# Kernel tuning notes

Measured on AMD Instinct MI355X. Metric: run time of the kernel, lower is better.

The kernel has to match this reference:

```python
import jax, jax.numpy as jnp
import numpy as np

N, DIM_EMB, HIDDEN, OUT = 8192, 256, 128, 64


def setup_inputs() -> dict:
    key = jax.random.key(0)
    k1, k2, k3, k4 = jax.random.split(key, 4)
    x = jax.random.normal(k1, (N, DIM_EMB), dtype=jnp.float32)
    adj = jax.random.uniform(k2, (N, N), dtype=jnp.float32)
    # GraphConvolution params (Glorot-style init)
    s1 = 1.0 / np.sqrt(DIM_EMB)
    s2 = 1.0 / np.sqrt(HIDDEN)
    W1 = jax.random.uniform(k3, (DIM_EMB, HIDDEN), dtype=jnp.float32, minval=-s1, maxval=s1)
    b1 = jnp.zeros((HIDDEN,), dtype=jnp.float32)
    W2 = jax.random.uniform(k4, (HIDDEN, OUT), dtype=jnp.float32, minval=-s2, maxval=s2)
    b2 = jnp.zeros((OUT,), dtype=jnp.float32)
    return {"x": x, "adj": adj, "W1": W1, "b1": b1, "W2": W2, "b2": b2}


def _adj_hat(adj):
    # torch: adj.mm(diag(d)).t().mm(diag(d)) == diag(d) @ adj.T @ diag(d)
    # expressed as broadcast row/col scaling (no NxN diag matmuls)
    d = jnp.power(jnp.sum(adj, axis=1), -0.5)  # [N]
    return (adj * d[None, :]).T * d[None, :]


def reference(x, adj, W1, b1, W2, b2):
    A = _adj_hat(adj)                     # [N, N]
    h = A @ (x @ W1) + b1                 # GraphConvolution 1
    h = jax.nn.relu(h)                    # dropout is identity in eval
    out = A @ (h @ W2) + b2               # GraphConvolution 2
    return out
```

## Files before the change

### kernel.cpp

```cpp
#include <hip/hip_runtime.h>
#include <math.h>

typedef unsigned short u16;
typedef __attribute__((ext_vector_type(8))) short short8v;
typedef __attribute__((ext_vector_type(4))) float f32x4v;
typedef __attribute__((ext_vector_type(4))) unsigned short u16x4;

#define GLOAD_LDS16(src, dst)                                      \
  __builtin_amdgcn_global_load_lds(                                \
      (const __attribute__((address_space(1))) void*)(src),        \
      (__attribute__((address_space(3))) void*)(dst), 16, 0, 0)

__device__ __forceinline__ u16 f2bf(float f) {
  union { float f; unsigned u; } v; v.f = f;
  unsigned r = v.u + 0x7FFFu + ((v.u >> 16) & 1u);
  return (u16)(r >> 16);
}

__global__ __launch_bounds__(256) void k_adj(const float* __restrict__ adj,
                                             u16* __restrict__ adjT,
                                             float* __restrict__ rsP) {
  __shared__ __align__(16) char Tsm[32768];
  const int tid = threadIdx.x, l = tid & 63, w = tid >> 6;
  const int c0 = blockIdx.x * 256, r0 = blockIdx.y * 64;
  for (int p = 0; p < 16; ++p) {
    const int rr = p * 4 + w;
    const float4 v = *(const float4*)(adj + (size_t)(r0 + rr) * 8192 + c0 + l * 4);
    float s = v.x + v.y + v.z + v.w;
#pragma unroll
    for (int off = 32; off > 0; off >>= 1) s += __shfl_xor(s, off, 64);
    if (l == 0) rsP[(size_t)blockIdx.x * 8192 + r0 + rr] = s;
    const float vv[4] = {v.x, v.y, v.z, v.w};
#pragma unroll
    for (int j = 0; j < 4; ++j) {
      const int c = l * 4 + j;
      const int phys = c * 128 + ((((rr >> 3) ^ (l & 7)) << 4) | ((rr & 7) << 1));
      *(u16*)(Tsm + phys) = f2bf(vv[j]);
    }
  }
  __syncthreads();
#pragma unroll
  for (int it = 0; it < 8; ++it) {
    const int chunk = it * 256 + tid;
    const int c = chunk >> 3, part = chunk & 7;
    const int pc = part ^ ((c >> 2) & 7);
    const float4 v = *(const float4*)(Tsm + c * 128 + pc * 16);
    *(float4*)((char*)adjT + ((size_t)(c0 + c) * 8192 + r0 + part * 8) * 2) = v;
  }
}

__global__ __launch_bounds__(256) void k_d(const float* __restrict__ rsP,
                                           float* __restrict__ dv) {
  const int i = blockIdx.x * 256 + threadIdx.x;
  float s = 0.f;
#pragma unroll
  for (int cx = 0; cx < 32; ++cx) s += rsP[(size_t)cx * 8192 + i];
  dv[i] = 1.0f / sqrtf(s);
}

__global__ __launch_bounds__(256) void k_prepw(const float* __restrict__ W1,
                                               const float* __restrict__ W2,
                                               u16* __restrict__ W1T,
                                               u16* __restrict__ W2T) {
  const int gid = blockIdx.x * 256 + threadIdx.x;
  { const int n = gid >> 8, c = gid & 255; W1T[gid] = f2bf(W1[c * 128 + n]); }
  if (gid < 8192) { const int n = gid >> 7, c = gid & 127; W2T[gid] = f2bf(W2[c * 64 + n]); }
}

__global__ __launch_bounds__(256) void k_convx(const float4* __restrict__ x,
                                               u16x4* __restrict__ xbf) {
  const int gid = blockIdx.x * 256 + threadIdx.x;
  const float4 v = x[gid];
  u16x4 o; o.x = f2bf(v.x); o.y = f2bf(v.y); o.z = f2bf(v.z); o.w = f2bf(v.w);
  xbf[gid] = o;
}

template <int BN, int EPI>
__global__ __launch_bounds__(256, 2) void gemm_kern(
    const u16* __restrict__ A, const u16* __restrict__ B,
    const float* __restrict__ dvec, float* __restrict__ Cp, u16* __restrict__ Ut,
    const int lda, const int ldb, const int ksteps) {
  constexpr int NREP = BN / 32;
  __shared__ __align__(16) u16 smem[16384 + 2 * BN * 64];
  const int tid = threadIdx.x, l = tid & 63, w = tid >> 6;
  const int wm = w >> 1, wn = w & 1;
  const int m0 = blockIdx.x * 128;
  const int kbase = blockIdx.y * ksteps * 64;
  const u16* Ag = A + (size_t)m0 * lda + kbase;
  const u16* Bg = B + kbase;
  u16* Asm = smem;
  u16* Bsm = smem + 16384;

  f32x4v acc[4][NREP];
  const f32x4v zero = {0.f, 0.f, 0.f, 0.f};
#pragma unroll
  for (int mr = 0; mr < 4; ++mr)
#pragma unroll
    for (int nr = 0; nr < NREP; ++nr) acc[mr][nr] = zero;

  auto stageA = [&](int k0, int buf) {
#pragma unroll
    for (int q = 0; q < 4; ++q) {
      const int c = q * 256 + tid;
      const int row = c >> 3;
      const int kp = (c & 7) ^ (row & 7);
      const u16* src = Ag + (size_t)row * lda + k0 + kp * 8;
      u16* dst = Asm + buf * 8192 + (q * 256 + (tid & ~63)) * 8;
      GLOAD_LDS16(src, dst);
    }
  };
  auto stageB = [&](int k0, int buf) {
#pragma unroll
    for (int q = 0; q < BN / 32; ++q) {
      const int c = q * 256 + tid;
      const int row = c >> 3;
      const int kp = (c & 7) ^ (row & 7);
      const u16* src = Bg + (size_t)row * ldb + k0 + kp * 8;
      u16* dst = Bsm + buf * (BN * 64) + (q * 256 + (tid & ~63)) * 8;
      GLOAD_LDS16(src, dst);
    }
  };

  stageA(0, 0);
  stageB(0, 0);

  for (int t = 0; t < ksteps; ++t) {
    const int cur = t & 1;
    __syncthreads();
    if (t + 1 < ksteps) { stageA((t + 1) * 64, cur ^ 1); stageB((t + 1) * 64, cur ^ 1); }
    const char* Ab = (const char*)(Asm + cur * 8192);
    const char* Bb = (const char*)(Bsm + cur * (BN * 64));
#pragma unroll
    for (int kk = 0; kk < 2; ++kk) {
      short8v a[4], b[NREP];
#pragma unroll
      for (int mr = 0; mr < 4; ++mr) {
        const int row = wm * 64 + mr * 16 + (l & 15);
        const int kb = kk * 64 + ((l >> 4) << 4);
        a[mr] = *(const short8v*)(Ab + row * 128 + (kb ^ ((row & 7) << 4)));
      }
#pragma unroll
      for (int nr = 0; nr < NREP; ++nr) {
        const int row = wn * (BN / 2) + nr * 16 + (l & 15);
        const int kb = kk * 64 + ((l >> 4) << 4);
        b[nr] = *(const short8v*)(Bb + row * 128 + (kb ^ ((row & 7) << 4)));
      }
#pragma unroll
      for (int mr = 0; mr < 4; ++mr)
#pragma unroll
        for (int nr = 0; nr < NREP; ++nr)
          acc[mr][nr] = __builtin_amdgcn_mfma_f32_16x16x32_bf16(a[mr], b[nr],
                                                                acc[mr][nr], 0, 0, 0);
    }
  }

  if (EPI == 0) {
    float* outp = Cp + (size_t)blockIdx.y * ((size_t)8192 * BN);
#pragma unroll
    for (int mr = 0; mr < 4; ++mr)
#pragma unroll
      for (int r = 0; r < 4; ++r) {
        const int m = m0 + wm * 64 + mr * 16 + ((l >> 4) << 2) + r;
#pragma unroll
        for (int nr = 0; nr < NREP; ++nr) {
          const int n = wn * (BN / 2) + nr * 16 + (l & 15);
          outp[(size_t)m * BN + n] = acc[mr][nr][r];
        }
      }
  } else {
    __syncthreads();
    u16* T = smem;
#pragma unroll
    for (int mr = 0; mr < 4; ++mr)
#pragma unroll
      for (int r = 0; r < 4; ++r) {
        const int mloc = wm * 64 + mr * 16 + ((l >> 4) << 2) + r;
        const float dd = dvec[m0 + mloc];
#pragma unroll
        for (int nr = 0; nr < NREP; ++nr) {
          const int n = wn * (BN / 2) + nr * 16 + (l & 15);
          T[n * 136 + mloc] = f2bf(acc[mr][nr][r] * dd);
        }
      }
    __syncthreads();
#pragma unroll
    for (int it = 0; it < BN / 16; ++it) {
      const int chunk = it * 256 + tid;
      const int n = chunk >> 4, part = chunk & 15;
      const float4 v = *(const float4*)(T + n * 136 + part * 8);
      *(float4*)((char*)Ut + ((size_t)n * 8192 + m0 + part * 8) * 2) = v;
    }
  }
}

__global__ __launch_bounds__(256) void k_e1(const float4* __restrict__ P,
                                            const float* __restrict__ dv,
                                            const float* __restrict__ b1,
                                            u16x4* __restrict__ h) {
  const int gid = blockIdx.x * 256 + threadIdx.x;
  const int STR = 262144;
  const float4 s0 = P[gid], s1 = P[gid + STR], s2 = P[gid + 2 * STR], s3 = P[gid + 3 * STR];
  const float dd = dv[gid >> 5];
  const float4 bb = ((const float4*)b1)[gid & 31];
  u16x4 o;
  o.x = f2bf(fmaxf(fmaf(dd, s0.x + s1.x + s2.x + s3.x, bb.x), 0.f));
  o.y = f2bf(fmaxf(fmaf(dd, s0.y + s1.y + s2.y + s3.y, bb.y), 0.f));
  o.z = f2bf(fmaxf(fmaf(dd, s0.z + s1.z + s2.z + s3.z, bb.z), 0.f));
  o.w = f2bf(fmaxf(fmaf(dd, s0.w + s1.w + s2.w + s3.w, bb.w), 0.f));
  h[gid] = o;
}

__global__ __launch_bounds__(256) void k_e2(const float4* __restrict__ P,
                                            const float* __restrict__ dv,
                                            const float* __restrict__ b2,
                                            float4* __restrict__ out) {
  const int gid = blockIdx.x * 256 + threadIdx.x;
  const int STR = 131072;
  const float4 s0 = P[gid], s1 = P[gid + STR], s2 = P[gid + 2 * STR], s3 = P[gid + 3 * STR];
  const float dd = dv[gid >> 4];
  const float4 bb = ((const float4*)b2)[gid & 15];
  float4 r;
  r.x = fmaf(dd, s0.x + s1.x + s2.x + s3.x, bb.x);
  r.y = fmaf(dd, s0.y + s1.y + s2.y + s3.y, bb.y);
  r.z = fmaf(dd, s0.z + s1.z + s2.z + s3.z, bb.z);
  r.w = fmaf(dd, s0.w + s1.w + s2.w + s3.w, bb.w);
  out[gid] = r;
}

extern "C" void kernel_launch(void* const* d_in, const int* in_sizes, int n_in,
                              void* d_out, int out_size, void* d_ws, size_t ws_size,
                              hipStream_t stream) {
  (void)in_sizes; (void)n_in; (void)out_size; (void)ws_size;
  const float* x   = (const float*)d_in[0];
  const float* adj = (const float*)d_in[1];
  const float* W1  = (const float*)d_in[2];
  const float* b1  = (const float*)d_in[3];
  const float* W2  = (const float*)d_in[4];
  const float* b2  = (const float*)d_in[5];
  float* out = (float*)d_out;
  char* ws = (char*)d_ws;

  u16*   adjT = (u16*)(ws + 0ull);
  float* T1p  = (float*)(ws + 134217728ull);
  float* T2p  = (float*)(ws + 151005184ull);
  u16*   xbf  = (u16*)(ws + 159393792ull);
  u16*   hbf  = (u16*)(ws + 163588096ull);
  u16*   U1T  = (u16*)(ws + 165685248ull);
  u16*   U2T  = (u16*)(ws + 167782400ull);
  u16*   W1T  = (u16*)(ws + 168830976ull);
  u16*   W2T  = (u16*)(ws + 168896512ull);
  float* rsP  = (float*)(ws + 168912896ull);
  float* dv   = (float*)(ws + 169961472ull);

  k_prepw<<<128, 256, 0, stream>>>(W1, W2, W1T, W2T);
  k_convx<<<2048, 256, 0, stream>>>((const float4*)x, (u16x4*)xbf);
  k_adj<<<dim3(32, 128), 256, 0, stream>>>(adj, adjT, rsP);
  k_d<<<32, 256, 0, stream>>>(rsP, dv);
  gemm_kern<128, 1><<<dim3(64, 1), 256, 0, stream>>>(xbf, W1T, dv, nullptr, U1T, 256, 256, 4);
  gemm_kern<128, 0><<<dim3(64, 4), 256, 0, stream>>>(adjT, U1T, nullptr, T1p, nullptr, 8192, 8192, 32);
  k_e1<<<1024, 256, 0, stream>>>((const float4*)T1p, dv, b1, (u16x4*)hbf);
  gemm_kern<64, 1><<<dim3(64, 1), 256, 0, stream>>>(hbf, W2T, dv, nullptr, U2T, 128, 128, 2);
  gemm_kern<64, 0><<<dim3(64, 4), 256, 0, stream>>>(adjT, U2T, nullptr, T2p, nullptr, 8192, 8192, 32);
  k_e2<<<512, 256, 0, stream>>>((const float4*)T2p, dv, b2, (float4*)out);
}
```

Baseline: 190.4 us.

## Shrink GEMM M-tile, batch adj loads, fuse prep kernels, reuse workspace

The GEMM kernel is templated on BM, and every launch now uses BM=64, which doubles the grid (128x4 instead of 64x4) to better fill the CUs at the cost of less A/B reuse per block. k_adj now issues 8 float4 loads before processing them, giving more memory-level parallelism. Its row-sum reduction is shortened to 16-lane groups, so partial sums grow to 128 slices, which k_d then reads. The weight-transpose and x-conversion kernels are merged into one launch, and the rsP buffer aliases T1p.

```diff
diff --git a/kernel.cpp b/kernel.cpp
--- a/kernel.cpp
+++ b/kernel.cpp
@@ -23,19 +23,30 @@
   __shared__ __align__(16) char Tsm[32768];
   const int tid = threadIdx.x, l = tid & 63, w = tid >> 6;
   const int c0 = blockIdx.x * 256, r0 = blockIdx.y * 64;
-  for (int p = 0; p < 16; ++p) {
-    const int rr = p * 4 + w;
-    const float4 v = *(const float4*)(adj + (size_t)(r0 + rr) * 8192 + c0 + l * 4);
-    float s = v.x + v.y + v.z + v.w;
-#pragma unroll
-    for (int off = 32; off > 0; off >>= 1) s += __shfl_xor(s, off, 64);
-    if (l == 0) rsP[(size_t)blockIdx.x * 8192 + r0 + rr] = s;
-    const float vv[4] = {v.x, v.y, v.z, v.w};
-#pragma unroll
-    for (int j = 0; j < 4; ++j) {
-      const int c = l * 4 + j;
-      const int phys = c * 128 + ((((rr >> 3) ^ (l & 7)) << 4) | ((rr & 7) << 1));
-      *(u16*)(Tsm + phys) = f2bf(vv[j]);
+  const int g = l >> 4;
+#pragma unroll
+  for (int pp = 0; pp < 2; ++pp) {
+    float4 v[8];
+#pragma unroll
+    for (int q = 0; q < 8; ++q) {
+      const int rr = (pp * 8 + q) * 4 + w;
+      v[q] = *(const float4*)(adj + (size_t)(r0 + rr) * 8192 + c0 + l * 4);
+    }
+#pragma unroll
+    for (int q = 0; q < 8; ++q) {
+      const int rr = (pp * 8 + q) * 4 + w;
+      float s = v[q].x + v[q].y + v[q].z + v[q].w;
+#pragma unroll
+      for (int off = 8; off > 0; off >>= 1) s += __shfl_xor(s, off, 64);
+      if ((l & 15) == 0)
+        rsP[(size_t)(blockIdx.x * 4 + g) * 8192 + r0 + rr] = s;
+      const float vv[4] = {v[q].x, v[q].y, v[q].z, v[q].w};
+#pragma unroll
+      for (int j = 0; j < 4; ++j) {
+        const int c = l * 4 + j;
+        const int phys = c * 128 + ((((rr >> 3) ^ (l & 7)) << 4) | ((rr & 7) << 1));
+        *(u16*)(Tsm + phys) = f2bf(vv[j]);
+      }
     }
   }
   __syncthreads();
@@ -53,59 +64,57 @@
                                            float* __restrict__ dv) {
   const int i = blockIdx.x * 256 + threadIdx.x;
   float s = 0.f;
-#pragma unroll
-  for (int cx = 0; cx < 32; ++cx) s += rsP[(size_t)cx * 8192 + i];
+#pragma unroll 8
+  for (int cx = 0; cx < 128; ++cx) s += rsP[(size_t)cx * 8192 + i];
   dv[i] = 1.0f / sqrtf(s);
 }
 
-__global__ __launch_bounds__(256) void k_prepw(const float* __restrict__ W1,
-                                               const float* __restrict__ W2,
-                                               u16* __restrict__ W1T,
-                                               u16* __restrict__ W2T) {
-  const int gid = blockIdx.x * 256 + threadIdx.x;
-  { const int n = gid >> 8, c = gid & 255; W1T[gid] = f2bf(W1[c * 128 + n]); }
-  if (gid < 8192) { const int n = gid >> 7, c = gid & 127; W2T[gid] = f2bf(W2[c * 64 + n]); }
-}
-
-__global__ __launch_bounds__(256) void k_convx(const float4* __restrict__ x,
-                                               u16x4* __restrict__ xbf) {
+__global__ __launch_bounds__(256) void k_prep(const float4* __restrict__ x,
+                                              u16x4* __restrict__ xbf,
+                                              const float* __restrict__ W1,
+                                              const float* __restrict__ W2,
+                                              u16* __restrict__ W1T,
+                                              u16* __restrict__ W2T) {
   const int gid = blockIdx.x * 256 + threadIdx.x;
   const float4 v = x[gid];
   u16x4 o; o.x = f2bf(v.x); o.y = f2bf(v.y); o.z = f2bf(v.z); o.w = f2bf(v.w);
   xbf[gid] = o;
-}
-
-template <int BN, int EPI>
+  if (gid < 32768) { const int n = gid >> 8, c = gid & 255; W1T[gid] = f2bf(W1[c * 128 + n]); }
+  if (gid < 8192)  { const int n = gid >> 7, c = gid & 127; W2T[gid] = f2bf(W2[c * 64 + n]); }
+}
+
+template <int BM, int BN, int EPI>
 __global__ __launch_bounds__(256, 2) void gemm_kern(
     const u16* __restrict__ A, const u16* __restrict__ B,
     const float* __restrict__ dvec, float* __restrict__ Cp, u16* __restrict__ Ut,
     const int lda, const int ldb, const int ksteps) {
+  constexpr int MREP = BM / 32;
   constexpr int NREP = BN / 32;
-  __shared__ __align__(16) u16 smem[16384 + 2 * BN * 64];
+  __shared__ __align__(16) u16 smem[2 * BM * 64 + 2 * BN * 64];
   const int tid = threadIdx.x, l = tid & 63, w = tid >> 6;
   const int wm = w >> 1, wn = w & 1;
-  const int m0 = blockIdx.x * 128;
+  const int m0 = blockIdx.x * BM;
   const int kbase = blockIdx.y * ksteps * 64;
   const u16* Ag = A + (size_t)m0 * lda + kbase;
   const u16* Bg = B + kbase;
   u16* Asm = smem;
-  u16* Bsm = smem + 16384;
-
-  f32x4v acc[4][NREP];
+  u16* Bsm = smem + 2 * BM * 64;
+
+  f32x4v acc[MREP][NREP];
   const f32x4v zero = {0.f, 0.f, 0.f, 0.f};
 #pragma unroll
-  for (int mr = 0; mr < 4; ++mr)
+  for (int mr = 0; mr < MREP; ++mr)
 #pragma unroll
     for (int nr = 0; nr < NREP; ++nr) acc[mr][nr] = zero;
 
   auto stageA = [&](int k0, int buf) {
 #pragma unroll
-    for (int q = 0; q < 4; ++q) {
+    for (int q = 0; q < BM / 32; ++q) {
       const int c = q * 256 + tid;
       const int row = c >> 3;
       const int kp = (c & 7) ^ (row & 7);
       const u16* src = Ag + (size_t)row * lda + k0 + kp * 8;
-      u16* dst = Asm + buf * 8192 + (q * 256 + (tid & ~63)) * 8;
+      u16* dst = Asm + buf * (BM * 64) + (q * 256 + (tid & ~63)) * 8;
       GLOAD_LDS16(src, dst);
     }
   };
@@ -128,14 +137,14 @@
     const int cur = t & 1;
     __syncthreads();
     if (t + 1 < ksteps) { stageA((t + 1) * 64, cur ^ 1); stageB((t + 1) * 64, cur ^ 1); }
-    const char* Ab = (const char*)(Asm + cur * 8192);
+    const char* Ab = (const char*)(Asm + cur * (BM * 64));
     const char* Bb = (const char*)(Bsm + cur * (BN * 64));
 #pragma unroll
     for (int kk = 0; kk < 2; ++kk) {
-      short8v a[4], b[NREP];
-#pragma unroll
-      for (int mr = 0; mr < 4; ++mr) {
-        const int row = wm * 64 + mr * 16 + (l & 15);
+      short8v a[MREP], b[NREP];
+#pragma unroll
+      for (int mr = 0; mr < MREP; ++mr) {
+        const int row = wm * (BM / 2) + mr * 16 + (l & 15);
         const int kb = kk * 64 + ((l >> 4) << 4);
         a[mr] = *(const short8v*)(Ab + row * 128 + (kb ^ ((row & 7) << 4)));
       }
@@ -146,7 +155,7 @@
         b[nr] = *(const short8v*)(Bb + row * 128 + (kb ^ ((row & 7) << 4)));
       }
 #pragma unroll
-      for (int mr = 0; mr < 4; ++mr)
+      for (int mr = 0; mr < MREP; ++mr)
 #pragma unroll
         for (int nr = 0; nr < NREP; ++nr)
           acc[mr][nr] = __builtin_amdgcn_mfma_f32_16x16x32_bf16(a[mr], b[nr],
@@ -157,10 +166,10 @@
   if (EPI == 0) {
     float* outp = Cp + (size_t)blockIdx.y * ((size_t)8192 * BN);
 #pragma unroll
-    for (int mr = 0; mr < 4; ++mr)
+    for (int mr = 0; mr < MREP; ++mr)
 #pragma unroll
       for (int r = 0; r < 4; ++r) {
-        const int m = m0 + wm * 64 + mr * 16 + ((l >> 4) << 2) + r;
+        const int m = m0 + wm * (BM / 2) + mr * 16 + ((l >> 4) << 2) + r;
 #pragma unroll
         for (int nr = 0; nr < NREP; ++nr) {
           const int n = wn * (BN / 2) + nr * 16 + (l & 15);
@@ -171,23 +180,23 @@
     __syncthreads();
     u16* T = smem;
 #pragma unroll
-    for (int mr = 0; mr < 4; ++mr)
+    for (int mr = 0; mr < MREP; ++mr)
 #pragma unroll
       for (int r = 0; r < 4; ++r) {
-        const int mloc = wm * 64 + mr * 16 + ((l >> 4) << 2) + r;
+        const int mloc = wm * (BM / 2) + mr * 16 + ((l >> 4) << 2) + r;
         const float dd = dvec[m0 + mloc];
 #pragma unroll
         for (int nr = 0; nr < NREP; ++nr) {
           const int n = wn * (BN / 2) + nr * 16 + (l & 15);
-          T[n * 136 + mloc] = f2bf(acc[mr][nr][r] * dd);
+          T[n * (BM + 8) + mloc] = f2bf(acc[mr][nr][r] * dd);
         }
       }
     __syncthreads();
 #pragma unroll
-    for (int it = 0; it < BN / 16; ++it) {
+    for (int it = 0; it < (BN * (BM / 8)) / 256; ++it) {
       const int chunk = it * 256 + tid;
-      const int n = chunk >> 4, part = chunk & 15;
-      const float4 v = *(const float4*)(T + n * 136 + part * 8);
+      const int n = chunk / (BM / 8), part = chunk & (BM / 8 - 1);
+      const float4 v = *(const float4*)(T + n * (BM + 8) + part * 8);
       *(float4*)((char*)Ut + ((size_t)n * 8192 + m0 + part * 8) * 2) = v;
     }
   }
@@ -249,17 +258,16 @@
   u16*   U2T  = (u16*)(ws + 167782400ull);
   u16*   W1T  = (u16*)(ws + 168830976ull);
   u16*   W2T  = (u16*)(ws + 168896512ull);
-  float* rsP  = (float*)(ws + 168912896ull);
-  float* dv   = (float*)(ws + 169961472ull);
-
-  k_prepw<<<128, 256, 0, stream>>>(W1, W2, W1T, W2T);
-  k_convx<<<2048, 256, 0, stream>>>((const float4*)x, (u16x4*)xbf);
+  float* dv   = (float*)(ws + 168912896ull);
+  float* rsP  = T1p;
+
+  k_prep<<<2048, 256, 0, stream>>>((const float4*)x, (u16x4*)xbf, W1, W2, W1T, W2T);
   k_adj<<<dim3(32, 128), 256, 0, stream>>>(adj, adjT, rsP);
   k_d<<<32, 256, 0, stream>>>(rsP, dv);
-  gemm_kern<128, 1><<<dim3(64, 1), 256, 0, stream>>>(xbf, W1T, dv, nullptr, U1T, 256, 256, 4);
-  gemm_kern<128, 0><<<dim3(64, 4), 256, 0, stream>>>(adjT, U1T, nullptr, T1p, nullptr, 8192, 8192, 32);
+  gemm_kern<64, 128, 1><<<dim3(128, 1), 256, 0, stream>>>(xbf, W1T, dv, nullptr, U1T, 256, 256, 4);
+  gemm_kern<64, 128, 0><<<dim3(128, 4), 256, 0, stream>>>(adjT, U1T, nullptr, T1p, nullptr, 8192, 8192, 32);
   k_e1<<<1024, 256, 0, stream>>>((const float4*)T1p, dv, b1, (u16x4*)hbf);
-  gemm_kern<64, 1><<<dim3(64, 1), 256, 0, stream>>>(hbf, W2T, dv, nullptr, U2T, 128, 128, 2);
-  gemm_kern<64, 0><<<dim3(64, 4), 256, 0, stream>>>(adjT, U2T, nullptr, T2p, nullptr, 8192, 8192, 32);
+  gemm_kern<64, 64, 1><<<dim3(128, 1), 256, 0, stream>>>(hbf, W2T, dv, nullptr, U2T, 128, 128, 2);
+  gemm_kern<64, 64, 0><<<dim3(128, 4), 256, 0, stream>>>(adjT, U2T, nullptr, T2p, nullptr, 8192, 8192, 32);
   k_e2<<<512, 256, 0, stream>>>((const float4*)T2p, dv, b2, (float4*)out);
 }
```

After: 182.7 us. 4.0% less time.
